# Kernel optimization log

Hardware: AMD Instinct MI355X
Metric: run time of the kernel (lower is better)

Reference implementation:

```python
import jax, jax.numpy as jnp
import numpy as np

BN_EPS = 1e-5


def setup_inputs() -> dict:
    key = jax.random.key(0)
    k1, k2 = jax.random.split(key)
    B, P, S, D = 8, 64, 256, 256
    x = jax.random.normal(k1, (B, P, S, D), dtype=jnp.float32)
    # kaiming_normal_ on (planes, S, S): std = sqrt(2 / fan_in), fan_in = S*S
    std = np.sqrt(2.0 / (S * S)).astype(np.float32)
    weights = jax.random.normal(k2, (P, S, S), dtype=jnp.float32) * std
    gamma = jnp.ones((P,), dtype=jnp.float32)
    beta = jnp.zeros((P,), dtype=jnp.float32)
    return {"x": x, "weights": weights, "gamma": gamma, "beta": beta}


def reference(x, weights, gamma, beta):
    # x: (B, P, S, D); weights: (P, S, S)
    D = x.shape[-1]
    inv_dim = 1.0 / jnp.sqrt(jnp.asarray(D, dtype=x.dtype))
    # scores: (B, P, S, S) = x @ x^T / sqrt(D)
    scores = jnp.einsum('bpsd,bptd->bpst', x, x) * inv_dim
    # weighted reduction over last axis -> (B, P, S, 1)
    red = jnp.sum(scores * weights[None], axis=-1, keepdims=True)
    y = x + red  # residual broadcast over D
    # BatchNorm2d in training mode: per-channel batch stats over (B, S, D)
    mean = jnp.mean(y, axis=(0, 2, 3), keepdims=True)
    var = jnp.var(y, axis=(0, 2, 3), keepdims=True)
    y_hat = (y - mean) * jax.lax.rsqrt(var + BN_EPS)
    return y_hat * gamma[None, :, None, None] + beta[None, :, None, None]
```

## Files before the change

### kernel.cpp

```cpp
#include <hip/hip_runtime.h>

typedef __attribute__((ext_vector_type(8))) short short8;
typedef __attribute__((ext_vector_type(4))) float f32x4;

#define NB 8
#define NP 64
#define NS 256
#define ND 256
#define LSTR 264

__device__ __forceinline__ unsigned short f2bf(float f) {
    unsigned int u = __float_as_uint(f);
    u = (u + 0x7FFFu + ((u >> 16) & 1u)) >> 16;
    return (unsigned short)u;
}

__global__ __launch_bounds__(1024, 4) void k1_gemm_red(
    const float* __restrict__ x, const float* __restrict__ w,
    float* __restrict__ red, float* __restrict__ Sx, float* __restrict__ Sxx)
{
    __shared__ unsigned short Xl[NS * LSTR];
    __shared__ float red_l[4][NS];

    const int t    = threadIdx.x;
    const int lane = t & 63;
    const int wv   = t >> 6;
    const int ib   = wv >> 2;
    const int jb   = wv & 3;
    const int p    = blockIdx.x & 63;
    const int b    = blockIdx.x >> 6;

    const float* xb      = x + (size_t)(b * NP + p) * (NS * ND);
    const size_t rowbase = (size_t)(b * NP + p) * NS;

    #pragma unroll 4
    for (int i = 0; i < 16; ++i) {
        const int row = 16 * i + wv;
        f32x4 v = *reinterpret_cast<const f32x4*>(xb + row * ND + 4 * lane);
        float a = (v.x + v.y) + (v.z + v.w);
        #pragma unroll
        for (int off = 1; off < 64; off <<= 1) a += __shfl_xor(a, off, 64);
        if (lane == 0) Sx[rowbase + row] = a;
        unsigned long long pk =
              (unsigned long long)f2bf(v.x)
            | ((unsigned long long)f2bf(v.y) << 16)
            | ((unsigned long long)f2bf(v.z) << 32)
            | ((unsigned long long)f2bf(v.w) << 48);
        *reinterpret_cast<unsigned long long*>(&Xl[row * LSTR + 4 * lane]) = pk;
    }
    __syncthreads();

    const int qd = lane >> 4;
    const int c  = lane & 15;

    f32x4 acc[4][4] = {};
    #pragma unroll 2
    for (int k0 = 0; k0 < ND; k0 += 32) {
        const int kof = k0 + qd * 8;
        short8 afr[4], bfr[4];
        #pragma unroll
        for (int i = 0; i < 4; ++i)
            afr[i] = *reinterpret_cast<const short8*>(
                &Xl[(64 * ib + 16 * i + c) * LSTR + kof]);
        #pragma unroll
        for (int j = 0; j < 4; ++j)
            bfr[j] = *reinterpret_cast<const short8*>(
                &Xl[(64 * jb + 16 * j + c) * LSTR + kof]);
        #pragma unroll
        for (int i = 0; i < 4; ++i)
            #pragma unroll
            for (int j = 0; j < 4; ++j)
                acc[i][j] = __builtin_amdgcn_mfma_f32_16x16x32_bf16(
                    afr[i], bfr[j], acc[i][j], 0, 0, 0);
    }

    if (ib == jb && qd == (c >> 2)) {
        #pragma unroll
        for (int i = 0; i < 4; ++i)
            Sxx[rowbase + 64 * ib + 16 * i + c] = acc[i][i][c & 3];
    }

    const float* wp = w + (size_t)p * (NS * NS);
    #pragma unroll
    for (int i = 0; i < 4; ++i) {
        #pragma unroll
        for (int r = 0; r < 4; ++r) {
            const int rl = 16 * i + 4 * qd + r;
            const float* wrow = wp + (size_t)(64 * ib + rl) * NS + 64 * jb + c;
            float s = acc[i][0][r] * wrow[0]
                    + acc[i][1][r] * wrow[16]
                    + acc[i][2][r] * wrow[32]
                    + acc[i][3][r] * wrow[48];
            #pragma unroll
            for (int off = 1; off < 16; off <<= 1)
                s += __shfl_xor(s, off, 64);
            if (c == 0) red_l[jb][64 * ib + rl] = s;
        }
    }
    __syncthreads();
    if (t < NS)
        red[rowbase + t] =
            (red_l[0][t] + red_l[1][t] + red_l[2][t] + red_l[3][t]) * 0.0625f;
}

__global__ __launch_bounds__(256) void k2_stats(
    const float* __restrict__ red, const float* __restrict__ Sx,
    const float* __restrict__ Sxx, const float* __restrict__ gamma,
    const float* __restrict__ beta, float* __restrict__ sb)
{
    __shared__ float l1[256], l2[256];
    const int p = blockIdx.x;
    const int t = threadIdx.x;
    float sy = 0.f, syy = 0.f;
    for (int n = t; n < NB * NS; n += 256) {
        int bb = n >> 8, s = n & 255;
        size_t idx = (size_t)(bb * NP + p) * NS + s;
        float r = red[idx], a = Sx[idx], q = Sxx[idx];
        sy  += a + 256.f * r;
        syy += q + 2.f * r * a + 256.f * r * r;
    }
    l1[t] = sy; l2[t] = syy;
    __syncthreads();
    for (int off = 128; off > 0; off >>= 1) {
        if (t < off) { l1[t] += l1[t + off]; l2[t] += l2[t + off]; }
        __syncthreads();
    }
    if (t == 0) {
        const float invN = 1.f / (float)(NB * NS * ND);
        float mean = l1[0] * invN;
        float var  = l2[0] * invN - mean * mean;
        float sc   = gamma[p] * rsqrtf(var + 1e-5f);
        sb[p]      = sc;
        sb[64 + p] = beta[p] - mean * sc;
    }
}

__global__ __launch_bounds__(256) void k3_norm(
    const float* __restrict__ x, const float* __restrict__ red,
    const float* __restrict__ sb, float* __restrict__ out)
{
    const size_t f0 = (size_t)blockIdx.x * 1024 + threadIdx.x;
    #pragma unroll
    for (int k = 0; k < 4; ++k) {
        const size_t f = f0 + (size_t)k * 256;
        f32x4 v = reinterpret_cast<const f32x4*>(x)[f];
        const float r  = red[f >> 6];
        const int   pp = (int)((f >> 14) & 63);
        v = (v + r) * sb[pp] + sb[64 + pp];
        reinterpret_cast<f32x4*>(out)[f] = v;
    }
}

extern "C" void kernel_launch(void* const* d_in, const int* in_sizes, int n_in,
                              void* d_out, int out_size, void* d_ws, size_t ws_size,
                              hipStream_t stream)
{
    const float* x     = (const float*)d_in[0];
    const float* w     = (const float*)d_in[1];
    const float* gamma = (const float*)d_in[2];
    const float* beta  = (const float*)d_in[3];
    float* out = (float*)d_out;

    float* red = (float*)d_ws;
    float* Sx  = red + (size_t)NB * NP * NS;
    float* Sxx = Sx  + (size_t)NB * NP * NS;
    float* sb  = Sxx + (size_t)NB * NP * NS;

    hipLaunchKernelGGL(k1_gemm_red, dim3(NB * NP), dim3(1024), 0, stream,
                       x, w, red, Sx, Sxx);
    hipLaunchKernelGGL(k2_stats, dim3(NP), dim3(256), 0, stream,
                       red, Sx, Sxx, gamma, beta, sb);
    hipLaunchKernelGGL(k3_norm, dim3((NB * NP * NS * ND) / (16 * 256)), dim3(256),
                       0, stream, x, red, sb, out);
}
```

Before: 289.7 us.

## Compute W·X GEMM per batch tile and dot with x rows

The row reduction is reassociated: instead of forming X·Xᵀ and weighting it by W, the kernel computes W·X in tiles over (p, row half, batch, column half) and takes the dot product of each result row with the fp32 x row. Partial results are accumulated with atomics into buffers zeroed by a new kernel. Sx and Sxx now come from exact fp32 x values in the epilogue rather than from the bf16 Gram diagonal. The aim is to replace the 1024-thread, large-LDS block with smaller 256-thread tiled blocks for better occupancy. The cost is that W is re-read for every batch, x is loaded as strided columns, there is no load/compute overlap, and both atomics and an extra launch are added.

```diff
diff --git a/kernel.cpp b/kernel.cpp
--- a/kernel.cpp
+++ b/kernel.cpp
@@ -7,7 +7,9 @@
 #define NP 64
 #define NS 256
 #define ND 256
-#define LSTR 264
+#define NH (NB * NP * NS)
+#define BK 32
+#define TSTR 40
 
 __device__ __forceinline__ unsigned short f2bf(float f) {
     unsigned int u = __float_as_uint(f);
@@ -15,92 +17,123 @@
     return (unsigned short)u;
 }
 
-__global__ __launch_bounds__(1024, 4) void k1_gemm_red(
+__global__ __launch_bounds__(256) void k0_zero(float* __restrict__ buf)
+{
+    const size_t i = (size_t)blockIdx.x * 1024 + threadIdx.x;
+    #pragma unroll
+    for (int k = 0; k < 4; ++k)
+        reinterpret_cast<f32x4*>(buf)[i + (size_t)k * 256] = f32x4{0.f, 0.f, 0.f, 0.f};
+}
+
+__global__ __launch_bounds__(256, 4) void k1_wx(
     const float* __restrict__ x, const float* __restrict__ w,
     float* __restrict__ red, float* __restrict__ Sx, float* __restrict__ Sxx)
 {
-    __shared__ unsigned short Xl[NS * LSTR];
-    __shared__ float red_l[4][NS];
+    __shared__ unsigned short Al[128 * TSTR];
+    __shared__ unsigned short Bl[128 * TSTR];
 
     const int t    = threadIdx.x;
     const int lane = t & 63;
-    const int wv   = t >> 6;
-    const int ib   = wv >> 2;
-    const int jb   = wv & 3;
-    const int p    = blockIdx.x & 63;
-    const int b    = blockIdx.x >> 6;
-
-    const float* xb      = x + (size_t)(b * NP + p) * (NS * ND);
-    const size_t rowbase = (size_t)(b * NP + p) * NS;
-
-    #pragma unroll 4
-    for (int i = 0; i < 16; ++i) {
-        const int row = 16 * i + wv;
-        f32x4 v = *reinterpret_cast<const f32x4*>(xb + row * ND + 4 * lane);
-        float a = (v.x + v.y) + (v.z + v.w);
-        #pragma unroll
-        for (int off = 1; off < 64; off <<= 1) a += __shfl_xor(a, off, 64);
-        if (lane == 0) Sx[rowbase + row] = a;
-        unsigned long long pk =
-              (unsigned long long)f2bf(v.x)
-            | ((unsigned long long)f2bf(v.y) << 16)
-            | ((unsigned long long)f2bf(v.z) << 32)
-            | ((unsigned long long)f2bf(v.w) << 48);
-        *reinterpret_cast<unsigned long long*>(&Xl[row * LSTR + 4 * lane]) = pk;
-    }
-    __syncthreads();
+    const int wq   = t >> 6;
+    const int qm   = wq >> 1;
+    const int qn   = wq & 1;
+    const int bid  = blockIdx.x;
+    const int p    = bid >> 5;
+    const int mt   = (bid >> 4) & 1;
+    const int nt   = bid & 15;
+    const int b    = nt >> 1;
+    const int d0   = (nt & 1) * 128;
+    const int Ms   = mt * 128;
+
+    const float* wp = w + (size_t)p * (NS * NS) + (size_t)Ms * NS;
+    const float* xb = x + (size_t)(b * NP + p) * (NS * ND);
+
+    const int ar  = t >> 1;
+    const int ak0 = (t & 1) * 16;
+    const int bn  = t & 127;
+    const int bk0 = (t >> 7) * 16;
 
     const int qd = lane >> 4;
     const int c  = lane & 15;
 
     f32x4 acc[4][4] = {};
-    #pragma unroll 2
-    for (int k0 = 0; k0 < ND; k0 += 32) {
-        const int kof = k0 + qd * 8;
-        short8 afr[4], bfr[4];
-        #pragma unroll
-        for (int i = 0; i < 4; ++i)
-            afr[i] = *reinterpret_cast<const short8*>(
-                &Xl[(64 * ib + 16 * i + c) * LSTR + kof]);
-        #pragma unroll
-        for (int j = 0; j < 4; ++j)
-            bfr[j] = *reinterpret_cast<const short8*>(
-                &Xl[(64 * jb + 16 * j + c) * LSTR + kof]);
-        #pragma unroll
-        for (int i = 0; i < 4; ++i)
+
+    for (int k0 = 0; k0 < NS; k0 += BK) {
+        {
+            const float* src = wp + (size_t)ar * NS + k0 + ak0;
+            #pragma unroll
+            for (int h = 0; h < 2; ++h) {
+                f32x4 v0 = *reinterpret_cast<const f32x4*>(src + 8 * h);
+                f32x4 v1 = *reinterpret_cast<const f32x4*>(src + 8 * h + 4);
+                short8 s8;
+                s8[0] = (short)f2bf(v0.x); s8[1] = (short)f2bf(v0.y);
+                s8[2] = (short)f2bf(v0.z); s8[3] = (short)f2bf(v0.w);
+                s8[4] = (short)f2bf(v1.x); s8[5] = (short)f2bf(v1.y);
+                s8[6] = (short)f2bf(v1.z); s8[7] = (short)f2bf(v1.w);
+                *reinterpret_cast<short8*>(&Al[ar * TSTR + ak0 + 8 * h]) = s8;
+            }
+        }
+        {
+            const float* src = xb + (size_t)(k0 + bk0) * ND + d0 + bn;
+            #pragma unroll
+            for (int h = 0; h < 2; ++h) {
+                short8 s8;
+                #pragma unroll
+                for (int j = 0; j < 8; ++j)
+                    s8[j] = (short)f2bf(src[(size_t)(8 * h + j) * ND]);
+                *reinterpret_cast<short8*>(&Bl[bn * TSTR + bk0 + 8 * h]) = s8;
+            }
+        }
+        __syncthreads();
+
+        {
+            const int kof = qd * 8;
+            short8 afr[4], bfr[4];
+            #pragma unroll
+            for (int i = 0; i < 4; ++i)
+                afr[i] = *reinterpret_cast<const short8*>(
+                    &Al[(64 * qm + 16 * i + c) * TSTR + kof]);
             #pragma unroll
             for (int j = 0; j < 4; ++j)
-                acc[i][j] = __builtin_amdgcn_mfma_f32_16x16x32_bf16(
-                    afr[i], bfr[j], acc[i][j], 0, 0, 0);
-    }
-
-    if (ib == jb && qd == (c >> 2)) {
-        #pragma unroll
-        for (int i = 0; i < 4; ++i)
-            Sxx[rowbase + 64 * ib + 16 * i + c] = acc[i][i][c & 3];
-    }
-
-    const float* wp = w + (size_t)p * (NS * NS);
+                bfr[j] = *reinterpret_cast<const short8*>(
+                    &Bl[(64 * qn + 16 * j + c) * TSTR + kof]);
+            #pragma unroll
+            for (int i = 0; i < 4; ++i)
+                #pragma unroll
+                for (int j = 0; j < 4; ++j)
+                    acc[i][j] = __builtin_amdgcn_mfma_f32_16x16x32_bf16(
+                        afr[i], bfr[j], acc[i][j], 0, 0, 0);
+        }
+        __syncthreads();
+    }
+
+    const float* xe = xb + (size_t)Ms * ND + d0;
+    const size_t rowbase = (size_t)(b * NP + p) * NS + Ms;
     #pragma unroll
     for (int i = 0; i < 4; ++i) {
         #pragma unroll
         for (int r = 0; r < 4; ++r) {
-            const int rl = 16 * i + 4 * qd + r;
-            const float* wrow = wp + (size_t)(64 * ib + rl) * NS + 64 * jb + c;
-            float s = acc[i][0][r] * wrow[0]
-                    + acc[i][1][r] * wrow[16]
-                    + acc[i][2][r] * wrow[32]
-                    + acc[i][3][r] * wrow[48];
-            #pragma unroll
-            for (int off = 1; off < 16; off <<= 1)
-                s += __shfl_xor(s, off, 64);
-            if (c == 0) red_l[jb][64 * ib + rl] = s;
-        }
-    }
-    __syncthreads();
-    if (t < NS)
-        red[rowbase + t] =
-            (red_l[0][t] + red_l[1][t] + red_l[2][t] + red_l[3][t]) * 0.0625f;
+            const int sl = 64 * qm + 16 * i + 4 * qd + r;
+            const float* xrow = xe + (size_t)sl * ND + 64 * qn + c;
+            const float x0 = xrow[0],  x1 = xrow[16];
+            const float x2 = xrow[32], x3 = xrow[48];
+            float pr = acc[i][0][r] * x0 + acc[i][1][r] * x1
+                     + acc[i][2][r] * x2 + acc[i][3][r] * x3;
+            float sx = (x0 + x1) + (x2 + x3);
+            float sq = (x0 * x0 + x1 * x1) + (x2 * x2 + x3 * x3);
+            #pragma unroll
+            for (int off = 1; off < 16; off <<= 1) {
+                pr += __shfl_xor(pr, off, 64);
+                sx += __shfl_xor(sx, off, 64);
+                sq += __shfl_xor(sq, off, 64);
+            }
+            if (c == 0) {
+                atomicAdd(&red[rowbase + sl], pr * 0.0625f);
+                atomicAdd(&Sx [rowbase + sl], sx);
+                atomicAdd(&Sxx[rowbase + sl], sq);
+            }
+        }
+    }
 }
 
 __global__ __launch_bounds__(256) void k2_stats(
@@ -162,11 +195,14 @@
     float* out = (float*)d_out;
 
     float* red = (float*)d_ws;
-    float* Sx  = red + (size_t)NB * NP * NS;
-    float* Sxx = Sx  + (size_t)NB * NP * NS;
-    float* sb  = Sxx + (size_t)NB * NP * NS;
-
-    hipLaunchKernelGGL(k1_gemm_red, dim3(NB * NP), dim3(1024), 0, stream,
+    float* Sx  = red + (size_t)NH;
+    float* Sxx = Sx  + (size_t)NH;
+    float* sb  = Sxx + (size_t)NH;
+
+    hipLaunchKernelGGL(k0_zero, dim3((3 * NH) / (4 * 1024)), dim3(256), 0, stream,
+                       red);
+
+    hipLaunchKernelGGL(k1_wx, dim3(NP * 32), dim3(256), 0, stream,
                        x, w, red, Sx, Sxx);
     hipLaunchKernelGGL(k2_stats, dim3(NP), dim3(256), 0, stream,
                        red, Sx, Sxx, gamma, beta, sb);
```

Result: slower. 311.1 us (+7.4%).
